# Performance work log

Hardware: AMD Instinct MI355X
Metric: run time of the kernel (lower is better)

The kernel has to match this reference:

```python
import jax, jax.numpy as jnp
import numpy as np

B, T, D = 2, 4096, 2048
HK, HV = 16, 32            # key heads, value heads (gqa_factor = 2)
AK, UV = 128, 128          # key head dim A, value head dim U
KEY_DIM = HK * AK          # 2048
VALUE_DIM = HV * UV        # 4096
CONV_DIM = 2 * KEY_DIM + VALUE_DIM  # 8192
KCONV = 4
CHUNK = 64
EPS = 1e-6


def setup_inputs() -> dict:
    key = jax.random.key(0)
    ks = jax.random.split(key, 10)
    s = lambda d: 1.0 / np.sqrt(d)
    return {
        "hidden": jax.random.normal(ks[0], (B, T, D), jnp.float32),
        "W_qkv": jax.random.normal(ks[1], (D, CONV_DIM), jnp.float32) * s(D),
        "W_z": jax.random.normal(ks[2], (D, VALUE_DIM), jnp.float32) * s(D),
        "W_b": jax.random.normal(ks[3], (D, HV), jnp.float32) * s(D),
        "W_a": jax.random.normal(ks[4], (D, HV), jnp.float32) * s(D),
        "conv_weight": jax.random.normal(ks[5], (CONV_DIM, KCONV), jnp.float32) * s(KCONV),
        "dt_bias": jnp.ones((HV,), jnp.float32),
        "A_log": jnp.log(jax.random.uniform(ks[6], (HV,), jnp.float32) * 16.0 + 1e-4),
        "norm_w": jnp.ones((UV,), jnp.float32),
        "W_out": jax.random.normal(ks[7], (VALUE_DIM, D), jnp.float32) * s(VALUE_DIM),
    }


def _l2norm(x, eps=1e-6):
    return x * jax.lax.rsqrt((x * x).sum(axis=-1, keepdims=True) + eps)


def _chunk_gated_delta_rule(q, k, v, g, beta, chunk_size=CHUNK):
    # inputs: q,k (B,T,Hv,A) l2-normalized below; v (B,T,Hv,U); g,beta (B,T,Hv)
    q = _l2norm(q)
    k = _l2norm(k)
    q, k, v = [x.transpose(0, 2, 1, 3).astype(jnp.float32) for x in (q, k, v)]
    beta = beta.transpose(0, 2, 1).astype(jnp.float32)
    g = g.transpose(0, 2, 1).astype(jnp.float32)
    Bs, H, Tt, A = k.shape
    U = v.shape[-1]
    pad = (chunk_size - Tt % chunk_size) % chunk_size
    if pad:
        q = jnp.pad(q, ((0, 0), (0, 0), (0, pad), (0, 0)))
        k = jnp.pad(k, ((0, 0), (0, 0), (0, pad), (0, 0)))
        v = jnp.pad(v, ((0, 0), (0, 0), (0, pad), (0, 0)))
        beta = jnp.pad(beta, ((0, 0), (0, 0), (0, pad)))
        g = jnp.pad(g, ((0, 0), (0, 0), (0, pad)))
    total = Tt + pad
    J = total // chunk_size
    q = q * (A ** -0.5)
    vb = v * beta[..., None]
    kb = k * beta[..., None]
    rs = lambda x, d: x.reshape(Bs, H, J, chunk_size, d)
    qj, kj, kbj = rs(q, A), rs(k, A), rs(kb, A)
    vbj = rs(vb, U)
    gj = jnp.cumsum(g.reshape(Bs, H, J, chunk_size), axis=-1)
    tril = jnp.tril(jnp.ones((chunk_size, chunk_size), jnp.float32))
    decay = jnp.exp((gj[..., :, None] - gj[..., None, :]) * tril) * tril
    upper = jnp.triu(jnp.ones((chunk_size, chunk_size), bool))
    attn = -(jnp.einsum('BHJLA,BHJMA->BHJLM', kbj, kj) * decay)
    attn = jnp.where(upper, 0.0, attn)

    def correction_step(i, a):  # sequential UT transform over rows
        row = a[..., i, :]
        return a.at[..., i, :].set(row + jnp.einsum('...j,...jk->...k', row, a))

    attn = jax.lax.fori_loop(1, chunk_size, correction_step, attn)
    attn = attn + jnp.eye(chunk_size, dtype=jnp.float32)
    v_corr = jnp.einsum('BHJLM,BHJMU->BHJLU', attn, vbj)
    k_cd = jnp.einsum('BHJLM,BHJMA->BHJLA', attn, kbj * jnp.exp(gj)[..., None])
    upper1 = jnp.triu(jnp.ones((chunk_size, chunk_size), bool), k=1)

    def chunk_step(st, j):  # st: (B,H,A,U) recurrent state
        qc, kc = qj[:, :, j], kj[:, :, j]
        vc, gc, kcd = v_corr[:, :, j], gj[:, :, j], k_cd[:, :, j]
        dm = decay[:, :, j]
        intra = jnp.einsum('BHLA,BHMA->BHLM', qc, kc) * dm
        intra = jnp.where(upper1, 0.0, intra)
        v_new = vc - jnp.einsum('BHLA,BHAU->BHLU', kcd, st)
        inter = jnp.exp(gc)[..., None] * jnp.einsum('BHLA,BHAU->BHLU', qc, st)
        out_c = inter + jnp.einsum('BHLM,BHMU->BHLU', intra, v_new)
        k_dec = kc * jnp.exp(gc[:, :, -1:] - gc)[..., None]
        st = st * jnp.exp(gc[:, :, -1])[..., None, None] + jnp.einsum('BHMA,BHMU->BHAU', k_dec, v_new)
        return st, out_c

    st0 = jnp.zeros((Bs, H, A, U), jnp.float32)
    _, outs = jax.lax.scan(chunk_step, st0, jnp.arange(J))
    out = outs.transpose(1, 2, 0, 3, 4).reshape(Bs, H, total, U)[:, :, :Tt]
    return out.transpose(0, 2, 1, 3)  # (B,T,H,U)


def _forward(hidden, W_qkv, W_z, W_b, W_a, conv_weight, dt_bias, A_log, norm_w, W_out):
    Bs, Tl, _ = hidden.shape
    mixed = (hidden @ W_qkv).transpose(0, 2, 1)  # (B, C, T)
    z = hidden @ W_z                              # (B, T, value_dim)
    b = hidden @ W_b                              # (B, T, Hv)
    a = hidden @ W_a                              # (B, T, Hv)
    # causal depthwise conv1d (kernel KCONV) + SiLU
    xp = jnp.pad(mixed, ((0, 0), (0, 0), (KCONV - 1, 0)))
    conv = sum(conv_weight[None, :, kk:kk + 1] * xp[:, :, kk:kk + Tl] for kk in range(KCONV))
    mixed = jax.nn.silu(conv).transpose(0, 2, 1)  # (B, T, C)
    q, k, v = jnp.split(mixed, [KEY_DIM, 2 * KEY_DIM], axis=-1)
    q = q.reshape(Bs, Tl, HK, AK)
    k = k.reshape(Bs, Tl, HK, AK)
    v = v.reshape(Bs, Tl, HV, UV)
    beta = jax.nn.sigmoid(b)
    g = -jnp.exp(A_log.astype(jnp.float32)) * jax.nn.softplus(a.astype(jnp.float32) + dt_bias)
    gqa = HV // HK
    q = jnp.repeat(q, gqa, axis=2)  # matches broadcast_to+reshape interleaving
    k = jnp.repeat(k, gqa, axis=2)
    core = _chunk_gated_delta_rule(q, k, v, g, beta)  # (B,T,Hv,U)
    # gated RMSNorm per value head (Mamba2/Qwen3-Next style: gate then norm)
    x = core.reshape(-1, UV)
    zf = z.reshape(-1, UV).astype(jnp.float32)
    xg = x * jax.nn.silu(zf)
    normed = norm_w * (xg * jax.lax.rsqrt((xg * xg).mean(-1, keepdims=True) + EPS))
    return normed.reshape(Bs, Tl, VALUE_DIM).astype(hidden.dtype) @ W_out


def reference(hidden, W_qkv, W_z, W_b, W_a, conv_weight, dt_bias, A_log, norm_w, W_out):
    return _forward(hidden, W_qkv, W_z, W_b, W_a, conv_weight, dt_bias, A_log, norm_w, W_out)
```

## Files before the change

kernel.cpp:

```cpp
#include <hip/hip_runtime.h>

#define B_   2
#define T_   4096
#define D_   2048
#define HV_  32
#define AK_  128
#define UV_  128
#define KD_  2048
#define VD_  4096
#define CD_  8192
#define CHK  64
#define NCH  (T_/CHK)

typedef __attribute__((ext_vector_type(4))) float  f32x4;
typedef __attribute__((ext_vector_type(8))) short  short8;
typedef __attribute__((ext_vector_type(4))) short  short4b;
typedef __attribute__((ext_vector_type(8))) unsigned short u16x8;
typedef __attribute__((ext_vector_type(4))) unsigned short u16x4;

__device__ __forceinline__ float bf2f(unsigned short u) {
  return __uint_as_float(((unsigned)u) << 16);
}
__device__ __forceinline__ unsigned short f2bf(float f) {
  unsigned u = __float_as_uint(f);
  return (unsigned short)((u + 0x7fffu + ((u >> 16) & 1u)) >> 16);
}
__device__ __forceinline__ void gload16(const void* g, void* l) {
  __builtin_amdgcn_global_load_lds((const __attribute__((address_space(1))) void*)g,
                                   (__attribute__((address_space(3))) void*)l, 16, 0, 0);
}

__global__ __launch_bounds__(256) void k_transpose(const float* __restrict__ src,
                                                   unsigned short* __restrict__ dst,
                                                   int K, int N) {
  __shared__ float tile[32][33];
  int k0 = blockIdx.x * 32, n0 = blockIdx.y * 32;
  int tx = threadIdx.x, ty = threadIdx.y;
  #pragma unroll
  for (int i = 0; i < 32; i += 8)
    tile[ty + i][tx] = src[(size_t)(k0 + ty + i) * N + n0 + tx];
  __syncthreads();
  #pragma unroll
  for (int i = 0; i < 32; i += 8)
    dst[(size_t)(n0 + ty + i) * K + k0 + tx] = f2bf(tile[tx][ty + i]);
}

__device__ __forceinline__ void storeC(float* p, float v) { *p = v; }
__device__ __forceinline__ void storeC(unsigned short* p, float v) { *p = f2bf(v); }

template <bool AGL, typename CT>
__global__ __launch_bounds__(256, 2) void k_gemm(const void* __restrict__ Av,
                                                 const unsigned short* __restrict__ BT,
                                                 CT* __restrict__ C, int N, int K) {
  __shared__ __attribute__((aligned(16))) short As[128 * 64];
  __shared__ __attribute__((aligned(16))) short Bs[256 * 64];
  const int tid  = threadIdx.x;
  const int bid  = blockIdx.x;
  const int tb   = bid & 63;
  const size_t bm = (size_t)(8 * (tb & 7) + (tb >> 3)) * 128;
  const size_t bn = (size_t)(bid >> 6) * 256;
  const int lane = tid & 63;
  const int wave = tid >> 6;
  const int wm = (wave >> 1) * 64;
  const int wn = (wave & 1) * 64;
  const int fr = lane & 15;
  const int kg = lane >> 4;
  const int lr = lane >> 3, lc8 = (lane & 7) * 8;
  const short* gb = (const short*)BT + (bn + wave * 64 + lr) * (size_t)K + lc8;
  short* lB = &Bs[wave * 64 * 64];
  const short* gab = (const short*)Av + (bm + wave * 32 + lr) * (size_t)K + lc8;
  short* lA = &As[wave * 32 * 64];

  f32x4 acc[4][8];
  #pragma unroll
  for (int i = 0; i < 4; ++i)
    #pragma unroll
    for (int j2 = 0; j2 < 8; ++j2) acc[i][j2] = (f32x4){0.f, 0.f, 0.f, 0.f};

  for (int kt = 0; kt < K; kt += 64) {
    __syncthreads();
    #pragma unroll
    for (int p = 0; p < 8; ++p)
      gload16(gb + kt + (size_t)(8 * p) * K, lB + (8 * p) * 64);
    if constexpr (AGL) {
      #pragma unroll
      for (int p = 0; p < 4; ++p)
        gload16(gab + kt + (size_t)(8 * p) * K, lA + (8 * p) * 64);
    } else {
      const float* Ag = (const float*)Av + bm * (size_t)K;
      #pragma unroll
      for (int s = 0; s < 8; ++s) {
        int ch = s * 256 + tid;
        int r = ch >> 4, c4 = (ch & 15) * 4;
        float4 v = *(const float4*)(Ag + (size_t)r * K + kt + c4);
        short4b sv = { (short)f2bf(v.x), (short)f2bf(v.y), (short)f2bf(v.z), (short)f2bf(v.w) };
        *(short4b*)&As[r * 64 + c4] = sv;
      }
    }
    __syncthreads();
    #pragma unroll
    for (int kk = 0; kk < 2; ++kk) {
      short8 af[4], bfr[8];
      #pragma unroll
      for (int mi = 0; mi < 4; ++mi) af[mi] = *(const short8*)&As[(wm + mi*16 + fr)*64 + kk*32 + kg*8];
      #pragma unroll
      for (int ni = 0; ni < 4; ++ni) {
        bfr[ni]     = *(const short8*)&Bs[(wn + ni*16 + fr)*64 + kk*32 + kg*8];
        bfr[4 + ni] = *(const short8*)&Bs[(128 + wn + ni*16 + fr)*64 + kk*32 + kg*8];
      }
      #pragma unroll
      for (int mi = 0; mi < 4; ++mi)
        #pragma unroll
        for (int ni = 0; ni < 8; ++ni)
          acc[mi][ni] = __builtin_amdgcn_mfma_f32_16x16x32_bf16(af[mi], bfr[ni], acc[mi][ni], 0, 0, 0);
    }
  }
  #pragma unroll
  for (int mi = 0; mi < 4; ++mi)
    #pragma unroll
    for (int ni = 0; ni < 8; ++ni) {
      size_t row = bm + wm + mi * 16 + kg * 4;
      size_t col = bn + (ni >= 4 ? 128 : 0) + wn + (ni & 3) * 16 + fr;
      #pragma unroll
      for (int e = 0; e < 4; ++e) storeC(&C[(row + e) * (size_t)N + col], acc[mi][ni][e]);
    }
}

__global__ __launch_bounds__(256) void k_beta_g(const float* __restrict__ hidden,
                                                const float* __restrict__ Wb,
                                                const float* __restrict__ Wa,
                                                const float* __restrict__ dt_bias,
                                                const float* __restrict__ A_log,
                                                float* __restrict__ betab,
                                                float* __restrict__ gbuf,
                                                unsigned short* __restrict__ hidb) {
  const int tid = threadIdx.x;
  const int r = tid >> 5, hh = tid & 31;
  const size_t bt = (size_t)blockIdx.x * 8 + r;
  const float* hrow = hidden + bt * D_;
  float sb = 0.f, sa = 0.f;
  for (int d = 0; d < D_; ++d) {
    float hv = hrow[d];
    sb += hv * Wb[d * 32 + hh];
    sa += hv * Wa[d * 32 + hh];
  }
  unsigned short* hb = hidb + bt * D_ + hh * 64;
  #pragma unroll
  for (int d2 = 0; d2 < 64; d2 += 8) {
    float4 v0 = *(const float4*)(hrow + hh * 64 + d2);
    float4 v1 = *(const float4*)(hrow + hh * 64 + d2 + 4);
    u16x8 o = { f2bf(v0.x), f2bf(v0.y), f2bf(v0.z), f2bf(v0.w),
                f2bf(v1.x), f2bf(v1.y), f2bf(v1.z), f2bf(v1.w) };
    *(u16x8*)(hb + d2) = o;
  }
  float beta = 1.f / (1.f + expf(-sb));
  float xg = sa + dt_bias[hh];
  float sp = (xg > 20.f) ? xg : log1pf(expf(xg));
  float g = -expf(A_log[hh]) * sp;
  int b = (int)(bt >> 12);
  int t = (int)(bt & (T_ - 1));
  size_t o = ((size_t)b * HV_ + hh) * T_ + t;
  betab[o] = beta;
  gbuf[o] = g;
}

__global__ __launch_bounds__(256) void k_qkv(const unsigned short* __restrict__ mqk,
                                             const float* __restrict__ cw,
                                             unsigned short* __restrict__ qn,
                                             unsigned short* __restrict__ kn) {
  const int row = blockIdx.x;
  const int b = row >> 12, t = row & (T_ - 1);
  const int tid = threadIdx.x;
  const int c0 = tid * 16;
  float4 w[16];
  #pragma unroll
  for (int e = 0; e < 16; ++e) w[e] = *(const float4*)&cw[(size_t)(c0 + e) * 4];
  float acc[16];
  #pragma unroll
  for (int e = 0; e < 16; ++e) acc[e] = 0.f;
  #pragma unroll
  for (int p = 0; p < 4; ++p) {
    int ts = t - 3 + p;
    if (ts < 0) continue;
    const unsigned short* src = mqk + (size_t)(b * T_ + ts) * 4096 + c0;
    u16x8 v0 = *(const u16x8*)src;
    u16x8 v1 = *(const u16x8*)(src + 8);
    #pragma unroll
    for (int e = 0; e < 8; ++e) {
      acc[e]     += bf2f(v0[e]) * ((const float*)&w[e])[p];
      acc[8 + e] += bf2f(v1[e]) * ((const float*)&w[8 + e])[p];
    }
  }
  float s = 0.f;
  #pragma unroll
  for (int e = 0; e < 16; ++e) {
    float x = acc[e];
    x = x / (1.f + expf(-x));
    acc[e] = x;
    s += x * x;
  }
  s += __shfl_xor(s, 1); s += __shfl_xor(s, 2); s += __shfl_xor(s, 4);
  float sc = rsqrtf(s + 1e-6f);
  bool isq = (c0 < KD_);
  if (isq) sc *= 0.08838834764831845f;
  int ch = isq ? c0 : (c0 - KD_);
  int hk = ch >> 7, cc = ch & 127;
  unsigned short* dst = (isq ? qn : kn) + ((size_t)(b * 16 + hk) * T_ + t) * 128 + cc;
  u16x8 o0, o1;
  #pragma unroll
  for (int e = 0; e < 8; ++e) { o0[e] = f2bf(acc[e] * sc); o1[e] = f2bf(acc[8 + e] * sc); }
  *(u16x8*)dst = o0;
  *(u16x8*)(dst + 8) = o1;
}

__global__ __launch_bounds__(256) void k_prep(const unsigned short* __restrict__ kn,
                                              const float* __restrict__ gbuf,
                                              const float* __restrict__ betab,
                                              unsigned short* __restrict__ Tg,
                                              unsigned short* __restrict__ knT,
                                              float* __restrict__ gjc) {
  __shared__ __attribute__((aligned(16))) unsigned short kl[CHK][136];
  __shared__ float L[CHK][65];
  __shared__ float W1[CHK][65];
  __shared__ float gj[CHK], bet[CHK];
  const int tid = threadIdx.x;
  const int blk = blockIdx.x;
  const int j = blk & 63, h = (blk >> 6) & 31, b = blk >> 11;
  const int hk = h >> 1;
  const int t0 = j * CHK;
  const int lane = tid & 63, wv = tid >> 6;
  const int fr = lane & 15, kg = lane >> 4;
  const int ty = tid >> 4, tx = tid & 15;

  const unsigned short* ksrc = kn + ((size_t)(b * 16 + hk) * T_ + t0) * 128;
  #pragma unroll
  for (int p = 0; p < 4; ++p) {
    int id = p * 256 + tid;
    int r = id >> 4, c = (id & 15) * 8;
    *(u16x8*)&kl[r][c] = *(const u16x8*)(ksrc + (size_t)r * 128 + c);
  }
  if (tid < 64) {
    float gval = gbuf[((size_t)b * HV_ + h) * T_ + t0 + tid];
    #pragma unroll
    for (int off = 1; off < 64; off <<= 1) {
      float o = __shfl_up(gval, off);
      if (tid >= off) gval += o;
    }
    gj[tid] = gval;
    gjc[((size_t)(b * HV_ + h) * NCH + j) * 64 + tid] = gval;
    bet[tid] = betab[((size_t)b * HV_ + h) * T_ + t0 + tid];
  }
  __syncthreads();

  if ((h & 1) == 0) {
    unsigned short* kd = knT + ((size_t)(b * 16 + hk) * NCH + j) * 8192;
    int a = tid >> 1, l0 = (tid & 1) * 32;
    u16x8 o[4];
    #pragma unroll
    for (int i = 0; i < 32; ++i) ((unsigned short*)o)[i] = kl[l0 + i][a];
    #pragma unroll
    for (int p = 0; p < 4; ++p) *(u16x8*)(kd + a * 64 + l0 + p * 8) = o[p];
  }

  {
    const int s0 = 16 * wv;
    f32x4 ag[4];
    #pragma unroll
    for (int mt = 0; mt < 4; ++mt) ag[mt] = (f32x4){0.f, 0.f, 0.f, 0.f};
    #pragma unroll
    for (int ks = 0; ks < 4; ++ks) {
      short8 af = *(const short8*)&kl[s0 + fr][ks * 32 + kg * 8];
      #pragma unroll
      for (int mt = 0; mt < 4; ++mt) {
        short8 bfv = *(const short8*)&kl[mt * 16 + fr][ks * 32 + kg * 8];
        ag[mt] = __builtin_amdgcn_mfma_f32_16x16x32_bf16(af, bfv, ag[mt], 0, 0, 0);
      }
    }
    #pragma unroll
    for (int mt = 0; mt < 4; ++mt)
      #pragma unroll
      for (int e = 0; e < 4; ++e) {
        int l = s0 + kg * 4 + e, m = mt * 16 + fr;
        L[l][m] = (l > m) ? (-bet[l] * ag[mt][e] * expf(gj[l] - gj[m])) : 0.f;
      }
  }
  __syncthreads();
  for (int i = tid; i < CHK * CHK; i += 256) { int l = i >> 6, m = i & 63; W1[l][m] = L[l][m]; }
  __syncthreads();

  #pragma unroll
  for (int dk = 1; dk <= 5; ++dk) {
    const int p2 = 1 << (dk - 1);
    float s4[4][4];
    #pragma unroll
    for (int i = 0; i < 4; ++i)
      #pragma unroll
      for (int c = 0; c < 4; ++c) s4[i][c] = 0.f;
    {
      const int hi = 16 * wv + 15 - p2;
      for (int jm = p2; jm <= hi; ++jm) {
        float wl[4], wr[4];
        #pragma unroll
        for (int i = 0; i < 4; ++i) wl[i] = W1[ty * 4 + i][jm];
        #pragma unroll
        for (int c = 0; c < 4; ++c) wr[c] = W1[jm][tx * 4 + c];
        #pragma unroll
        for (int i = 0; i < 4; ++i)
          #pragma unroll
          for (int c = 0; c < 4; ++c) s4[i][c] += wl[i] * wr[c];
      }
    }
    __syncthreads();
    #pragma unroll
    for (int i = 0; i < 4; ++i)
      #pragma unroll
      for (int c = 0; c < 4; ++c) W1[ty * 4 + i][tx * 4 + c] = s4[i][c];
    __syncthreads();
    float pu[4][4];
    #pragma unroll
    for (int i = 0; i < 4; ++i)
      #pragma unroll
      for (int c = 0; c < 4; ++c) pu[i][c] = L[ty * 4 + i][tx * 4 + c] + W1[ty * 4 + i][tx * 4 + c];
    {
      const int hi = 16 * wv + 14;
      for (int jm = p2 * 2; jm <= hi; ++jm) {
        float pl[4], wr[4];
        #pragma unroll
        for (int i = 0; i < 4; ++i) pl[i] = L[ty * 4 + i][jm];
        #pragma unroll
        for (int c = 0; c < 4; ++c) wr[c] = W1[jm][tx * 4 + c];
        #pragma unroll
        for (int i = 0; i < 4; ++i)
          #pragma unroll
          for (int c = 0; c < 4; ++c) pu[i][c] += pl[i] * wr[c];
      }
    }
    __syncthreads();
    #pragma unroll
    for (int i = 0; i < 4; ++i)
      #pragma unroll
      for (int c = 0; c < 4; ++c) L[ty * 4 + i][tx * 4 + c] = pu[i][c];
    __syncthreads();
  }
  unsigned short* td = Tg + (size_t)blk * 4096;
  #pragma unroll
  for (int pp = 0; pp < 2; ++pp) {
    int id = pp * 256 + tid;
    int l = id >> 3, m8 = (id & 7) * 8;
    u16x8 o;
    #pragma unroll
    for (int e = 0; e < 8; ++e) {
      float v = L[l][m8 + e] + ((l == m8 + e) ? 1.f : 0.f);
      o[e] = f2bf(v);
    }
    *(u16x8*)(td + (size_t)l * 64 + m8) = o;
  }
}

__global__ __launch_bounds__(256) void k_scan(const unsigned short* __restrict__ qn,
                                              const unsigned short* __restrict__ kn,
                                              const unsigned short* __restrict__ mv,
                                              const unsigned short* __restrict__ Tg,
                                              const unsigned short* __restrict__ knT,
                                              const float* __restrict__ gjc,
                                              const float* __restrict__ betab,
                                              const float* __restrict__ cw,
                                              unsigned short* __restrict__ xout) {
  __shared__ __attribute__((aligned(16))) unsigned short kl[CHK][136], ql[CHK][136];
  __shared__ __attribute__((aligned(16))) unsigned short Ubuf[9216];
  __shared__ float ST[16][132];
  __shared__ __attribute__((aligned(16))) unsigned short SbT[16][136];
  __shared__ __attribute__((aligned(16))) unsigned short vbT[16][72], vnT[16][72], vndT[16][72];
  __shared__ float gj[CHK], bet[CHK], eg[CHK], edec[CHK], beg[CHK];

  unsigned short (*Tl)[72]   = (unsigned short(*)[72])(&Ubuf[0]);
  unsigned short (*intr)[72] = (unsigned short(*)[72])(&Ubuf[4608]);

  const int tid = threadIdx.x;
  const int blk = blockIdx.x;
  const int xcd  = blk & 7;
  const int slot = blk >> 3;
  const int g    = xcd + 8 * (slot >> 4);
  const int wgrp = slot & 15;
  const int b  = g >> 4;
  const int hk = g & 15;
  const int h  = hk * 2 + (wgrp >> 3);
  const int us = wgrp & 7;
  const int u0 = us * 16;
  const int lane = tid & 63, wv = tid >> 6;
  const int fr = lane & 15, kg = lane >> 4;
  const int s0 = 16 * wv;

  const int cvl = tid >> 2, c4 = (tid & 3) * 4;
  float4 wv4[4];
  #pragma unroll
  for (int i = 0; i < 4; ++i)
    wv4[i] = *(const float4*)&cw[(size_t)(2 * KD_ + h * 128 + u0 + c4 + i) * 4];

  for (int i = tid; i < 16 * 132; i += 256) (&ST[0][0])[i] = 0.f;

  const unsigned short* qsrc = qn + (size_t)(b * 16 + hk) * T_ * 128;
  const unsigned short* ksrc = kn + (size_t)(b * 16 + hk) * T_ * 128;
  const unsigned short* tsrc = Tg + (size_t)((b * 32 + h) * 64) * 4096;
  const unsigned short* knsrc = knT + (size_t)(b * 16 + hk) * NCH * 8192;
  const float* gsrc = gjc + (size_t)(b * 32 + h) * 4096;
  const float* bsrc = betab + ((size_t)b * HV_ + h) * T_;

  const int rr = tid >> 4, cc8 = (tid & 15) * 8;
  const int tr = tid >> 3, tc8 = (tid & 7) * 8;

  u16x8 krg[4], qrg[4], trg[2];
  u16x4 vld[4];
  float g_r = 0.f, b_r = 0.f;

  #pragma unroll
  for (int p = 0; p < 4; ++p) {
    int r = p * 16 + rr;
    krg[p] = *(const u16x8*)(ksrc + (size_t)r * 128 + cc8);
    qrg[p] = *(const u16x8*)(qsrc + (size_t)r * 128 + cc8);
  }
  #pragma unroll
  for (int p = 0; p < 2; ++p) {
    int r = p * 32 + tr;
    trg[p] = *(const u16x8*)(tsrc + (size_t)r * 64 + tc8);
  }
  if (tid < 64) { g_r = gsrc[tid]; b_r = bsrc[tid]; }
  #pragma unroll
  for (int p = 0; p < 4; ++p) {
    int ts = cvl - 3 + p;
    vld[p] = (ts >= 0) ? *(const u16x4*)(mv + (size_t)(b * T_ + ts) * 4096 + h * 128 + u0 + c4)
                       : (u16x4){0, 0, 0, 0};
  }
  #pragma unroll
  for (int p = 0; p < 4; ++p) {
    int r = p * 16 + rr;
    *(u16x8*)&kl[r][cc8] = krg[p];
    *(u16x8*)&ql[r][cc8] = qrg[p];
  }
  #pragma unroll
  for (int p = 0; p < 2; ++p) {
    int r = p * 32 + tr;
    *(u16x8*)&Tl[r][tc8] = trg[p];
  }
  if (tid < 64) { gj[tid] = g_r; bet[tid] = b_r; }
  __syncthreads();

  for (int j = 0; j < NCH; ++j) {
    const int t0 = j * CHK;
    short8 kr[2][2];
    #pragma unroll
    for (int t2 = 0; t2 < 2; ++t2) {
      int a0 = wv * 32 + t2 * 16;
      #pragma unroll
      for (int ks = 0; ks < 2; ++ks)
        kr[t2][ks] = *(const short8*)(knsrc + (size_t)j * 8192 + (a0 + fr) * 64 + ks * 32 + kg * 8);
    }
    if (j + 1 < NCH) {
      const int t1 = t0 + CHK;
      #pragma unroll
      for (int p = 0; p < 4; ++p) {
        int r = p * 16 + rr;
        krg[p] = *(const u16x8*)(ksrc + (size_t)(t1 + r) * 128 + cc8);
        qrg[p] = *(const u16x8*)(qsrc + (size_t)(t1 + r) * 128 + cc8);
      }
      #pragma unroll
      for (int p = 0; p < 2; ++p) {
        int r = p * 32 + tr;
        trg[p] = *(const u16x8*)(tsrc + (size_t)(j + 1) * 4096 + r * 64 + tc8);
      }
      if (tid < 64) { g_r = gsrc[(j + 1) * 64 + tid]; b_r = bsrc[t1 + tid]; }
    }
    if (tid < 64) {
      float gl = gj[63];
      float e = expf(gj[tid]);
      eg[tid] = e;
      edec[tid] = expf(gl - gj[tid]);
      beg[tid] = bet[tid] * e;
    }
    {
      float a4[4] = {0.f, 0.f, 0.f, 0.f};
      #pragma unroll
      for (int p = 0; p < 4; ++p)
        #pragma unroll
        for (int i = 0; i < 4; ++i) a4[i] += bf2f(vld[p][i]) * ((const float*)&wv4[i])[p];
      float be = bet[cvl];
      #pragma unroll
      for (int i = 0; i < 4; ++i) {
        float x = a4[i];
        x = x / (1.f + expf(-x)) * be;
        vbT[c4 + i][cvl] = f2bf(x);
      }
    }
    if (j + 1 < NCH) {
      #pragma unroll
      for (int p = 0; p < 4; ++p) {
        int ts = t0 + CHK + cvl - 3 + p;
        vld[p] = *(const u16x4*)(mv + (size_t)(b * T_ + ts) * 4096 + h * 128 + u0 + c4);
      }
    }
    {
      int u = tid >> 4, a8 = (tid & 15) * 8;
      u16x8 o;
      #pragma unroll
      for (int e = 0; e < 8; ++e) o[e] = f2bf(ST[u][a8 + e]);
      *(u16x8*)&SbT[u][a8] = o;
    }
    __syncthreads();

    {
      f32x4 ag[4];
      #pragma unroll
      for (int mt = 0; mt < 4; ++mt) ag[mt] = (f32x4){0.f, 0.f, 0.f, 0.f};
      #pragma unroll
      for (int ks = 0; ks < 4; ++ks) {
        short8 af = *(const short8*)&ql[s0 + fr][ks * 32 + kg * 8];
        #pragma unroll
        for (int mt = 0; mt < 4; ++mt) {
          short8 bfv = *(const short8*)&kl[mt * 16 + fr][ks * 32 + kg * 8];
          ag[mt] = __builtin_amdgcn_mfma_f32_16x16x32_bf16(af, bfv, ag[mt], 0, 0, 0);
        }
      }
      #pragma unroll
      for (int mt = 0; mt < 4; ++mt)
        #pragma unroll
        for (int e = 0; e < 4; ++e) {
          int l = s0 + kg * 4 + e, m = mt * 16 + fr;
          float v = (l >= m) ? (ag[mt][e] * expf(gj[l] - gj[m])) : 0.f;
          intr[l][m] = f2bf(v);
        }
    }
    {
      f32x4 a1 = (f32x4){0.f, 0.f, 0.f, 0.f};
      #pragma unroll
      for (int ks = 0; ks < 4; ++ks) {
        short8 af = *(const short8*)&kl[s0 + fr][ks * 32 + kg * 8];
        short8 bfv = *(const short8*)&SbT[fr][ks * 32 + kg * 8];
        a1 = __builtin_amdgcn_mfma_f32_16x16x32_bf16(af, bfv, a1, 0, 0, 0);
      }
      #pragma unroll
      for (int e = 0; e < 4; ++e) {
        int l = s0 + kg * 4 + e;
        float vm = bf2f(vbT[fr][l]) - beg[l] * a1[e];
        vbT[fr][l] = f2bf(vm);
      }
    }
    __syncthreads();
    {
      f32x4 a2 = (f32x4){0.f, 0.f, 0.f, 0.f};
      #pragma unroll
      for (int ks = 0; ks < 2; ++ks) {
        short8 af = *(const short8*)&Tl[s0 + fr][ks * 32 + kg * 8];
        short8 bfv = *(const short8*)&vbT[fr][ks * 32 + kg * 8];
        a2 = __builtin_amdgcn_mfma_f32_16x16x32_bf16(af, bfv, a2, 0, 0, 0);
      }
      #pragma unroll
      for (int e = 0; e < 4; ++e) {
        int l = s0 + kg * 4 + e;
        vnT[fr][l]  = f2bf(a2[e]);
        vndT[fr][l] = f2bf(a2[e] * edec[l]);
      }
    }
    __syncthreads();
    {
      f32x4 ai = (f32x4){0.f, 0.f, 0.f, 0.f};
      f32x4 aq = (f32x4){0.f, 0.f, 0.f, 0.f};
      #pragma unroll
      for (int ks = 0; ks < 2; ++ks) {
        short8 af = *(const short8*)&intr[s0 + fr][ks * 32 + kg * 8];
        short8 bfv = *(const short8*)&vnT[fr][ks * 32 + kg * 8];
        ai = __builtin_amdgcn_mfma_f32_16x16x32_bf16(af, bfv, ai, 0, 0, 0);
      }
      #pragma unroll
      for (int ks = 0; ks < 4; ++ks) {
        short8 af = *(const short8*)&ql[s0 + fr][ks * 32 + kg * 8];
        short8 bfv = *(const short8*)&SbT[fr][ks * 32 + kg * 8];
        aq = __builtin_amdgcn_mfma_f32_16x16x32_bf16(af, bfv, aq, 0, 0, 0);
      }
      #pragma unroll
      for (int e = 0; e < 4; ++e) {
        int l = s0 + kg * 4 + e;
        float o = eg[l] * aq[e] + ai[e];
        xout[((size_t)(b * T_ + t0 + l) * HV_ + h) * UV_ + u0 + fr] = f2bf(o);
      }
    }
    {
      float egl = eg[63];
      #pragma unroll
      for (int t2 = 0; t2 < 2; ++t2) {
        int a0 = wv * 32 + t2 * 16;
        f32x4 cf;
        #pragma unroll
        for (int e = 0; e < 4; ++e) cf[e] = ST[kg * 4 + e][a0 + fr] * egl;
        #pragma unroll
        for (int ks = 0; ks < 2; ++ks) {
          short8 af = *(const short8*)&vndT[fr][ks * 32 + kg * 8];
          cf = __builtin_amdgcn_mfma_f32_16x16x32_bf16(af, kr[t2][ks], cf, 0, 0, 0);
        }
        #pragma unroll
        for (int e = 0; e < 4; ++e) ST[kg * 4 + e][a0 + fr] = cf[e];
      }
    }
    __syncthreads();
    if (j + 1 < NCH) {
      #pragma unroll
      for (int p = 0; p < 4; ++p) {
        int r = p * 16 + rr;
        *(u16x8*)&kl[r][cc8] = krg[p];
        *(u16x8*)&ql[r][cc8] = qrg[p];
      }
      #pragma unroll
      for (int p = 0; p < 2; ++p) {
        int r = p * 32 + tr;
        *(u16x8*)&Tl[r][tc8] = trg[p];
      }
      if (tid < 64) { gj[tid] = g_r; bet[tid] = b_r; }
    }
    __syncthreads();
  }
}

__global__ __launch_bounds__(256) void k_gate_norm(const unsigned short* __restrict__ x,
                                                   const unsigned short* __restrict__ z,
                                                   const float* __restrict__ nw,
                                                   unsigned short* __restrict__ out) {
  const int row = blockIdx.x * 4 + (threadIdx.x >> 6);
  const int lane = threadIdx.x & 63;
  const unsigned short* xp = x + (size_t)row * UV_;
  const unsigned short* zp = z + (size_t)row * UV_;
  float x0 = bf2f(xp[lane]), x1 = bf2f(xp[lane + 64]);
  float z0 = bf2f(zp[lane]), z1 = bf2f(zp[lane + 64]);
  float g0 = x0 * (z0 / (1.f + expf(-z0)));
  float g1 = x1 * (z1 / (1.f + expf(-z1)));
  float s = g0 * g0 + g1 * g1;
  #pragma unroll
  for (int off = 32; off > 0; off >>= 1) s += __shfl_xor(s, off);
  float r = rsqrtf(s * (1.f / UV_) + 1e-6f);
  out[(size_t)row * UV_ + lane]      = f2bf(nw[lane] * g0 * r);
  out[(size_t)row * UV_ + lane + 64] = f2bf(nw[lane + 64] * g1 * r);
}

extern "C" void kernel_launch(void* const* d_in, const int* in_sizes, int n_in,
                              void* d_out, int out_size, void* d_ws, size_t ws_size,
                              hipStream_t stream) {
  (void)in_sizes; (void)n_in; (void)out_size; (void)ws_size;
  const float* hidden  = (const float*)d_in[0];
  const float* W_qkv   = (const float*)d_in[1];
  const float* W_z     = (const float*)d_in[2];
  const float* W_b     = (const float*)d_in[3];
  const float* W_a     = (const float*)d_in[4];
  const float* conv_w  = (const float*)d_in[5];
  const float* dt_bias = (const float*)d_in[6];
  const float* A_log   = (const float*)d_in[7];
  const float* norm_w  = (const float*)d_in[8];
  const float* W_out   = (const float*)d_in[9];
  float* out = (float*)d_out;

  const size_t MB = 1048576ull;
  char* w = (char*)d_ws;
  unsigned short* wqkvT = (unsigned short*)(w);
  unsigned short* Tg    = (unsigned short*)(w);
  unsigned short* mqk   = (unsigned short*)(w + 32 * MB);
  unsigned short* xcore = (unsigned short*)(w + 32 * MB);
  unsigned short* mv    = (unsigned short*)(w + 96 * MB);
  unsigned short* normed= (unsigned short*)(w + 96 * MB);
  unsigned short* hidb  = (unsigned short*)(w + 160 * MB);
  unsigned short* qn    = (unsigned short*)(w + 160 * MB);
  unsigned short* zb    = (unsigned short*)(w + 160 * MB);
  unsigned short* knT   = (unsigned short*)(w + 192 * MB);
  unsigned short* kn    = (unsigned short*)(w + 224 * MB);
  unsigned short* wzT   = (unsigned short*)(w + 224 * MB);
  unsigned short* woutT = (unsigned short*)(w + 240 * MB);
  float*          betab = (float*)(w + 288 * MB);
  float*          gbuf  = (float*)(w + 289 * MB);
  float*          gjc   = (float*)(w + 290 * MB);

  k_beta_g<<<dim3(B_ * T_ / 8), 256, 0, stream>>>(hidden, W_b, W_a, dt_bias, A_log, betab, gbuf, hidb);
  k_transpose<<<dim3(D_ / 32, CD_ / 32), dim3(32, 8), 0, stream>>>(W_qkv, wqkvT, D_, CD_);
  k_gemm<true, unsigned short><<<dim3(64 * 16), 256, 0, stream>>>(hidb, wqkvT, mqk, 4096, 2048);
  k_gemm<true, unsigned short><<<dim3(64 * 16), 256, 0, stream>>>(hidb, wqkvT + (size_t)4096 * 2048, mv, 4096, 2048);
  k_qkv<<<dim3(B_ * T_), 256, 0, stream>>>(mqk, conv_w, qn, kn);
  k_prep<<<dim3(B_ * HV_ * NCH), 256, 0, stream>>>(kn, gbuf, betab, Tg, knT, gjc);
  k_scan<<<dim3(B_ * HV_ * 8), 256, 0, stream>>>(qn, kn, mv, Tg, knT, gjc, betab, conv_w, xcore);
  k_transpose<<<dim3(D_ / 32, VD_ / 32), dim3(32, 8), 0, stream>>>(W_z, wzT, D_, VD_);
  k_gemm<false, unsigned short><<<dim3(64 * 16), 256, 0, stream>>>(hidden, wzT, zb, 4096, 2048);
  k_transpose<<<dim3(VD_ / 32, D_ / 32), dim3(32, 8), 0, stream>>>(W_out, woutT, VD_, D_);
  k_gate_norm<<<dim3(B_ * T_ * HV_ / 4), 256, 0, stream>>>(xcore, zb, norm_w, normed);
  k_gemm<true, float><<<dim3(64 * 8), 256, 0, stream>>>(normed, woutT, out, 2048, 4096);
}
```

Baseline: 1.662 ms.

## Double-buffer GEMM K-loop and rebalance row mapping in triangular inverse kernel

The GEMM kernel moves from a single 64-wide K tile with two barriers per iteration to double-buffered 32-wide tiles. The next tile's global loads are issued (and the fp32 A operand is staged in registers) while MFMAs run on the current tile, leaving one barrier per step. The chunk inverse kernel now gives each thread rows interleaved by 16 instead of 4 contiguous rows. This evens out triangular work across waves, at the cost of per-row guard branches inside the inner loop. Halving the K tile doubles the number of iterations and barriers.

```diff
diff --git a/kernel.cpp b/kernel.cpp
--- a/kernel.cpp
+++ b/kernel.cpp
@@ -52,8 +52,8 @@
 __global__ __launch_bounds__(256, 2) void k_gemm(const void* __restrict__ Av,
                                                  const unsigned short* __restrict__ BT,
                                                  CT* __restrict__ C, int N, int K) {
-  __shared__ __attribute__((aligned(16))) short As[128 * 64];
-  __shared__ __attribute__((aligned(16))) short Bs[256 * 64];
+  __shared__ __attribute__((aligned(16))) short As[2][128 * 32];
+  __shared__ __attribute__((aligned(16))) short Bs[2][256 * 32];
   const int tid  = threadIdx.x;
   const int bid  = blockIdx.x;
   const int tb   = bid & 63;
@@ -65,11 +65,11 @@
   const int wn = (wave & 1) * 64;
   const int fr = lane & 15;
   const int kg = lane >> 4;
-  const int lr = lane >> 3, lc8 = (lane & 7) * 8;
-  const short* gb = (const short*)BT + (bn + wave * 64 + lr) * (size_t)K + lc8;
-  short* lB = &Bs[wave * 64 * 64];
+  const int lr = lane >> 2, lc8 = (lane & 3) * 8;
+  const short* gb  = (const short*)BT + (bn + wave * 64 + lr) * (size_t)K + lc8;
   const short* gab = (const short*)Av + (bm + wave * 32 + lr) * (size_t)K + lc8;
-  short* lA = &As[wave * 32 * 64];
+  const float* Agf = (const float*)Av + (bm + (tid >> 3)) * (size_t)K + (tid & 7) * 4;
+  const int ar = tid >> 3, ac4 = (tid & 7) * 4;
 
   f32x4 acc[4][8];
   #pragma unroll
@@ -77,43 +77,65 @@
     #pragma unroll
     for (int j2 = 0; j2 < 8; ++j2) acc[i][j2] = (f32x4){0.f, 0.f, 0.f, 0.f};
 
-  for (int kt = 0; kt < K; kt += 64) {
-    __syncthreads();
-    #pragma unroll
-    for (int p = 0; p < 8; ++p)
-      gload16(gb + kt + (size_t)(8 * p) * K, lB + (8 * p) * 64);
-    if constexpr (AGL) {
+  #pragma unroll
+  for (int p = 0; p < 4; ++p)
+    gload16(gb + (size_t)(16 * p) * K, &Bs[0][(wave * 64 + 16 * p) * 32]);
+  if constexpr (AGL) {
+    #pragma unroll
+    for (int p = 0; p < 2; ++p)
+      gload16(gab + (size_t)(16 * p) * K, &As[0][(wave * 32 + 16 * p) * 32]);
+  } else {
+    #pragma unroll
+    for (int s = 0; s < 4; ++s) {
+      float4 v = *(const float4*)(Agf + (size_t)(32 * s) * K);
+      short4b sv = { (short)f2bf(v.x), (short)f2bf(v.y), (short)f2bf(v.z), (short)f2bf(v.w) };
+      *(short4b*)&As[0][(ar + 32 * s) * 32 + ac4] = sv;
+    }
+  }
+  __syncthreads();
+
+  int cur = 0;
+  for (int kt = 0; kt < K; kt += 32, cur ^= 1) {
+    const bool nxt = (kt + 32) < K;
+    float4 va[4];
+    if (nxt) {
       #pragma unroll
       for (int p = 0; p < 4; ++p)
-        gload16(gab + kt + (size_t)(8 * p) * K, lA + (8 * p) * 64);
-    } else {
-      const float* Ag = (const float*)Av + bm * (size_t)K;
-      #pragma unroll
-      for (int s = 0; s < 8; ++s) {
-        int ch = s * 256 + tid;
-        int r = ch >> 4, c4 = (ch & 15) * 4;
-        float4 v = *(const float4*)(Ag + (size_t)r * K + kt + c4);
-        short4b sv = { (short)f2bf(v.x), (short)f2bf(v.y), (short)f2bf(v.z), (short)f2bf(v.w) };
-        *(short4b*)&As[r * 64 + c4] = sv;
-      }
-    }
-    __syncthreads();
-    #pragma unroll
-    for (int kk = 0; kk < 2; ++kk) {
-      short8 af[4], bfr[8];
-      #pragma unroll
-      for (int mi = 0; mi < 4; ++mi) af[mi] = *(const short8*)&As[(wm + mi*16 + fr)*64 + kk*32 + kg*8];
-      #pragma unroll
-      for (int ni = 0; ni < 4; ++ni) {
-        bfr[ni]     = *(const short8*)&Bs[(wn + ni*16 + fr)*64 + kk*32 + kg*8];
-        bfr[4 + ni] = *(const short8*)&Bs[(128 + wn + ni*16 + fr)*64 + kk*32 + kg*8];
-      }
-      #pragma unroll
-      for (int mi = 0; mi < 4; ++mi)
-        #pragma unroll
-        for (int ni = 0; ni < 8; ++ni)
-          acc[mi][ni] = __builtin_amdgcn_mfma_f32_16x16x32_bf16(af[mi], bfr[ni], acc[mi][ni], 0, 0, 0);
-    }
+        gload16(gb + kt + 32 + (size_t)(16 * p) * K, &Bs[cur ^ 1][(wave * 64 + 16 * p) * 32]);
+      if constexpr (AGL) {
+        #pragma unroll
+        for (int p = 0; p < 2; ++p)
+          gload16(gab + kt + 32 + (size_t)(16 * p) * K, &As[cur ^ 1][(wave * 32 + 16 * p) * 32]);
+      } else {
+        #pragma unroll
+        for (int s = 0; s < 4; ++s)
+          va[s] = *(const float4*)(Agf + (size_t)(32 * s) * K + kt + 32);
+      }
+    }
+    short8 af[4], bfr[8];
+    #pragma unroll
+    for (int mi = 0; mi < 4; ++mi) af[mi] = *(const short8*)&As[cur][(wm + mi*16 + fr)*32 + kg*8];
+    #pragma unroll
+    for (int ni = 0; ni < 4; ++ni) {
+      bfr[ni]     = *(const short8*)&Bs[cur][(wn + ni*16 + fr)*32 + kg*8];
+      bfr[4 + ni] = *(const short8*)&Bs[cur][(128 + wn + ni*16 + fr)*32 + kg*8];
+    }
+    #pragma unroll
+    for (int mi = 0; mi < 4; ++mi)
+      #pragma unroll
+      for (int ni = 0; ni < 8; ++ni)
+        acc[mi][ni] = __builtin_amdgcn_mfma_f32_16x16x32_bf16(af[mi], bfr[ni], acc[mi][ni], 0, 0, 0);
+    if constexpr (!AGL) {
+      if (nxt) {
+        #pragma unroll
+        for (int s = 0; s < 4; ++s) {
+          short4b sv = { (short)f2bf(va[s].x), (short)f2bf(va[s].y),
+                         (short)f2bf(va[s].z), (short)f2bf(va[s].w) };
+          *(short4b*)&As[cur ^ 1][(ar + 32 * s) * 32 + ac4] = sv;
+        }
+      }
+    }
+    __syncthreads();
   }
   #pragma unroll
   for (int mi = 0; mi < 4; ++mi)
@@ -297,49 +319,53 @@
       #pragma unroll
       for (int c = 0; c < 4; ++c) s4[i][c] = 0.f;
     {
-      const int hi = 16 * wv + 15 - p2;
-      for (int jm = p2; jm <= hi; ++jm) {
-        float wl[4], wr[4];
-        #pragma unroll
-        for (int i = 0; i < 4; ++i) wl[i] = W1[ty * 4 + i][jm];
+      const int hiA = 4 * wv + 51 - p2;
+      for (int jm = p2; jm <= hiA; ++jm) {
+        float wr[4];
         #pragma unroll
         for (int c = 0; c < 4; ++c) wr[c] = W1[jm][tx * 4 + c];
         #pragma unroll
-        for (int i = 0; i < 4; ++i)
-          #pragma unroll
-          for (int c = 0; c < 4; ++c) s4[i][c] += wl[i] * wr[c];
+        for (int i = 0; i < 4; ++i) {
+          if (jm <= 4 * wv + 3 + 16 * i - p2) {
+            float wl = W1[ty + 16 * i][jm];
+            #pragma unroll
+            for (int c = 0; c < 4; ++c) s4[i][c] += wl * wr[c];
+          }
+        }
       }
     }
     __syncthreads();
     #pragma unroll
     for (int i = 0; i < 4; ++i)
       #pragma unroll
-      for (int c = 0; c < 4; ++c) W1[ty * 4 + i][tx * 4 + c] = s4[i][c];
+      for (int c = 0; c < 4; ++c) W1[ty + 16 * i][tx * 4 + c] = s4[i][c];
     __syncthreads();
     float pu[4][4];
     #pragma unroll
     for (int i = 0; i < 4; ++i)
       #pragma unroll
-      for (int c = 0; c < 4; ++c) pu[i][c] = L[ty * 4 + i][tx * 4 + c] + W1[ty * 4 + i][tx * 4 + c];
-    {
-      const int hi = 16 * wv + 14;
-      for (int jm = p2 * 2; jm <= hi; ++jm) {
-        float pl[4], wr[4];
-        #pragma unroll
-        for (int i = 0; i < 4; ++i) pl[i] = L[ty * 4 + i][jm];
+      for (int c = 0; c < 4; ++c) pu[i][c] = L[ty + 16 * i][tx * 4 + c] + W1[ty + 16 * i][tx * 4 + c];
+    {
+      const int hiB = 4 * wv + 50;
+      for (int jm = p2 * 2; jm <= hiB; ++jm) {
+        float wr[4];
         #pragma unroll
         for (int c = 0; c < 4; ++c) wr[c] = W1[jm][tx * 4 + c];
         #pragma unroll
-        for (int i = 0; i < 4; ++i)
-          #pragma unroll
-          for (int c = 0; c < 4; ++c) pu[i][c] += pl[i] * wr[c];
+        for (int i = 0; i < 4; ++i) {
+          if (jm <= 4 * wv + 2 + 16 * i) {
+            float pl = L[ty + 16 * i][jm];
+            #pragma unroll
+            for (int c = 0; c < 4; ++c) pu[i][c] += pl * wr[c];
+          }
+        }
       }
     }
     __syncthreads();
     #pragma unroll
     for (int i = 0; i < 4; ++i)
       #pragma unroll
-      for (int c = 0; c < 4; ++c) L[ty * 4 + i][tx * 4 + c] = pu[i][c];
+      for (int c = 0; c < 4; ++c) L[ty + 16 * i][tx * 4 + c] = pu[i][c];
     __syncthreads();
   }
   unsigned short* td = Tg + (size_t)blk * 4096;
```

New measurement: 1.861 ms. 1.12x slower.
